# Kernel tuning notes

Measured on AMD Instinct MI355X. Metric: run time of the kernel, lower is better.

Reference implementation:

```python
import jax, jax.numpy as jnp
import numpy as np

L, D, H, N = 9, 256, 4, 1024
DH = D // H          # head dim = 64
FH = DH // 2         # fourier half dim = 32


def _lin(x, W, b):
    return x @ W + b


def _ln(x, g, b, eps=1e-5):
    mu = jnp.mean(x, -1, keepdims=True)
    var = jnp.mean((x - mu) ** 2, -1, keepdims=True)
    return (x - mu) * jax.lax.rsqrt(var + eps) * g + b


def _ffn(x, m, W1, b1, g, beta, W2, b2):
    h = jax.nn.gelu(_ln(_lin(jnp.concatenate([x, m], -1), W1, b1), g, beta), approximate=False)
    return x + _lin(h, W2, b2)


def _rotate_half(x):
    x1, x2 = x[..., 0::2], x[..., 1::2]
    return jnp.stack((-x2, x1), -1).reshape(x.shape)


def _rope(f, t):
    return t * f[0] + _rotate_half(t) * f[1]


def _posenc(kpts, Wr):
    proj = kpts @ Wr                                   # [b,n,FH]
    emb = jnp.stack([jnp.cos(proj), jnp.sin(proj)], 0)  # [2,b,n,FH]
    emb = jnp.repeat(emb, 2, axis=3)                    # [2,b,n,DH]
    return emb[:, None]                                 # [2,1,b,n,DH]


def _heads(t):
    b, n, _ = t.shape
    return t.reshape(b, n, H, DH).transpose(0, 2, 1, 3)


def _merge(t):
    b, h, n, d = t.shape
    return t.transpose(0, 2, 1, 3).reshape(b, n, h * d)


def _self_block(x, enc, Wqkv, bqkv, Wo, bo, fp):
    b, n, _ = x.shape
    qkv = _lin(x, Wqkv, bqkv).reshape(b, n, H, DH, 3).transpose(0, 2, 1, 3, 4)
    q, k, v = qkv[..., 0], qkv[..., 1], qkv[..., 2]
    q, k = _rope(enc, q), _rope(enc, k)
    attn = jax.nn.softmax(jnp.einsum('bhid,bhjd->bhij', q, k) * DH ** -0.5, -1)
    msg = _lin(_merge(jnp.einsum('bhij,bhjd->bhid', attn, v)), Wo, bo)
    return _ffn(x, msg, *fp)


def _cross_block(x0, x1, Wqk, bqk, Wv, bv, Wo, bo, fp):
    s = DH ** -0.25
    qk0 = _heads(_lin(x0, Wqk, bqk)) * s
    qk1 = _heads(_lin(x1, Wqk, bqk)) * s
    v0, v1 = _heads(_lin(x0, Wv, bv)), _heads(_lin(x1, Wv, bv))
    sim = jnp.einsum('bhid,bhjd->bhij', qk0, qk1)       # shared similarity
    m0 = jnp.einsum('bhij,bhjd->bhid', jax.nn.softmax(sim, -1), v1)
    m1 = jnp.einsum('bhij,bhid->bhjd', jax.nn.softmax(sim, -2), v0)
    m0, m1 = _lin(_merge(m0), Wo, bo), _lin(_merge(m1), Wo, bo)
    return _ffn(x0, m0, *fp), _ffn(x1, m1, *fp)


def _assignment(d0, d1, Wp, bp, Wz, bz):
    s = D ** -0.25
    md0, md1 = _lin(d0, Wp, bp) * s, _lin(d1, Wp, bp) * s
    sim = jnp.einsum('bmd,bnd->bmn', md0, md1)
    z0 = d0 @ Wz + bz[:1]                               # [b,m,1]
    z1 = d1 @ Wz + bz[:1]                               # [b,n,1]
    cert = jax.nn.log_sigmoid(z0) + jnp.swapaxes(jax.nn.log_sigmoid(z1), 1, 2)
    inner = jax.nn.log_softmax(sim, -1) + jax.nn.log_softmax(sim, -2) + cert
    col = jax.nn.log_sigmoid(-z0)                       # [b,m,1]
    row = jnp.swapaxes(jax.nn.log_sigmoid(-z1), 1, 2)   # [b,1,n]
    top = jnp.concatenate([inner, col], 2)
    bot = jnp.concatenate([row, jnp.zeros_like(row[:, :, :1])], 2)
    return jnp.concatenate([top, bot], 1)               # [b,m+1,n+1]


def _forward(desc0, desc1, kpts0, kpts1, Wr,
             sWqkv, sbqkv, sWo, sbo, sfW1, sfb1, sfg, sfbeta, sfW2, sfb2,
             cWqk, cbqk, cWv, cbv, cWo, cbo, cfW1, cfb1, cfg, cfbeta, cfW2, cfb2,
             mWp, mbp, mWz, mbz):
    enc0, enc1 = _posenc(kpts0, Wr), _posenc(kpts1, Wr)
    for i in range(L):
        sfp = (sfW1[i], sfb1[i], sfg[i], sfbeta[i], sfW2[i], sfb2[i])
        cfp = (cfW1[i], cfb1[i], cfg[i], cfbeta[i], cfW2[i], cfb2[i])
        desc0 = _self_block(desc0, enc0, sWqkv[i], sbqkv[i], sWo[i], sbo[i], sfp)
        desc1 = _self_block(desc1, enc1, sWqkv[i], sbqkv[i], sWo[i], sbo[i], sfp)
        desc0, desc1 = _cross_block(desc0, desc1, cWqk[i], cbqk[i], cWv[i], cbv[i], cWo[i], cbo[i], cfp)
    return _assignment(desc0, desc1, mWp, mbp, mWz, mbz)


def setup_inputs() -> dict:
    key = jax.random.key(0)
    ks = iter(jax.random.split(key, 64))

    def nrm(shape, std=0.02):
        return std * jax.random.normal(next(ks), shape, jnp.float32)

    return {
        'desc0': nrm((1, N, D), 1.0), 'desc1': nrm((1, N, D), 1.0),
        'kpts0': nrm((1, N, 2), 1.0), 'kpts1': nrm((1, N, 2), 1.0),
        'Wr': nrm((2, FH), 1.0),
        'sWqkv': nrm((L, D, 3 * D)), 'sbqkv': jnp.zeros((L, 3 * D), jnp.float32),
        'sWo': nrm((L, D, D)), 'sbo': jnp.zeros((L, D), jnp.float32),
        'sfW1': nrm((L, 2 * D, 2 * D)), 'sfb1': jnp.zeros((L, 2 * D), jnp.float32),
        'sfg': jnp.ones((L, 2 * D), jnp.float32), 'sfbeta': jnp.zeros((L, 2 * D), jnp.float32),
        'sfW2': nrm((L, 2 * D, D)), 'sfb2': jnp.zeros((L, D), jnp.float32),
        'cWqk': nrm((L, D, D)), 'cbqk': jnp.zeros((L, D), jnp.float32),
        'cWv': nrm((L, D, D)), 'cbv': jnp.zeros((L, D), jnp.float32),
        'cWo': nrm((L, D, D)), 'cbo': jnp.zeros((L, D), jnp.float32),
        'cfW1': nrm((L, 2 * D, 2 * D)), 'cfb1': jnp.zeros((L, 2 * D), jnp.float32),
        'cfg': jnp.ones((L, 2 * D), jnp.float32), 'cfbeta': jnp.zeros((L, 2 * D), jnp.float32),
        'cfW2': nrm((L, 2 * D, D)), 'cfb2': jnp.zeros((L, D), jnp.float32),
        'mWp': nrm((D, D)), 'mbp': jnp.zeros((D,), jnp.float32),
        'mWz': nrm((D, 1)), 'mbz': jnp.zeros((D,), jnp.float32),
    }


def reference(desc0, desc1, kpts0, kpts1, Wr,
              sWqkv, sbqkv, sWo, sbo, sfW1, sfb1, sfg, sfbeta, sfW2, sfb2,
              cWqk, cbqk, cWv, cbv, cWo, cbo, cfW1, cfb1, cfg, cfbeta, cfW2, cfb2,
              mWp, mbp, mWz, mbz):
    return _forward(desc0, desc1, kpts0, kpts1, Wr,
                    sWqkv, sbqkv, sWo, sbo, sfW1, sfb1, sfg, sfbeta, sfW2, sfb2,
                    cWqk, cbqk, cWv, cbv, cWo, cbo, cfW1, cfb1, cfg, cfbeta, cfW2, cfb2,
                    mWp, mbp, mWz, mbz)
```

## Files before the change

kernel.cpp:

```cpp
#include <hip/hip_runtime.h>
#include <cmath>

#define NTOK 1024
#define DM   256
#define NH   4
#define DH   64
#define NL   9

typedef __attribute__((ext_vector_type(8))) __bf16 bf16x8;
typedef __attribute__((ext_vector_type(4))) __bf16 bf16x4;
typedef __attribute__((ext_vector_type(4))) float  f32x4;

__device__ __forceinline__ float logsigf(float x) {
    return fminf(x, 0.0f) - log1pf(expf(-fabsf(x)));
}

__device__ __forceinline__ __bf16 f2bf(float f) {
    unsigned u = __float_as_uint(f);
    u = (u + 0x7FFFu + ((u >> 16) & 1u)) >> 16;
    unsigned short s = (unsigned short)u;
    return __builtin_bit_cast(__bf16, s);
}

__global__ __launch_bounds__(256) void wtrans_all_k(
    const float* __restrict__ sWqkv, const float* __restrict__ sWo,
    const float* __restrict__ sfW1,  const float* __restrict__ sfW2,
    const float* __restrict__ cWqk,  const float* __restrict__ cWv,
    const float* __restrict__ cWo,   const float* __restrict__ cfW1,
    const float* __restrict__ cfW2,  const float* __restrict__ mWp,
    __bf16* __restrict__ wb)
{
    const int z = blockIdx.z;
    const float* src; __bf16* dst; int K, N, b;
    if      (z <  9) { src = sWqkv; dst = wb;            K = 256; N = 768; b = z;      }
    else if (z < 18) { src = sWo;   dst = wb + 1769472;  K = 256; N = 256; b = z - 9;  }
    else if (z < 27) { src = sfW1;  dst = wb + 2359296;  K = 512; N = 512; b = z - 18; }
    else if (z < 36) { src = sfW2;  dst = wb + 4718592;  K = 512; N = 256; b = z - 27; }
    else if (z < 45) { src = cWqk;  dst = wb + 5898240;  K = 256; N = 256; b = z - 36; }
    else if (z < 54) { src = cWv;   dst = wb + 6488064;  K = 256; N = 256; b = z - 45; }
    else if (z < 63) { src = cWo;   dst = wb + 7077888;  K = 256; N = 256; b = z - 54; }
    else if (z < 72) { src = cfW1;  dst = wb + 7667712;  K = 512; N = 512; b = z - 63; }
    else if (z < 81) { src = cfW2;  dst = wb + 10027008; K = 512; N = 256; b = z - 72; }
    else             { src = mWp;   dst = wb + 11206656; K = 256; N = 256; b = 0;      }
    const int n0 = blockIdx.x * 32, k0 = blockIdx.y * 32;
    if (n0 >= N || k0 >= K) return;
    src += (size_t)b * K * N;
    dst += (size_t)b * K * N;

    __shared__ __bf16 t[32][36];
    const int tx = threadIdx.x & 31, ty = threadIdx.x >> 5;
    #pragma unroll
    for (int i = 0; i < 4; ++i) {
        int k = ty + i * 8;
        t[tx][k] = f2bf(src[(size_t)(k0 + k) * N + n0 + tx]);
    }
    __syncthreads();
    const int nr = threadIdx.x >> 3, kc = (threadIdx.x & 7) * 4;
    bf16x4 v = *(const bf16x4*)&t[nr][kc];
    int outr = n0 + nr;
    if (z < 9) {
        int h = outr / 192, r = outr % 192;
        outr = (r % 3) * 256 + h * 64 + (r / 3);
    }
    *(bf16x4*)&dst[(size_t)outr * K + k0 + kc] = v;
}

__global__ __launch_bounds__(256) void wfuse_k(
    const __bf16* __restrict__ tW1s, const __bf16* __restrict__ tWos,
    const __bf16* __restrict__ tW1c, const __bf16* __restrict__ tWoc,
    __bf16* __restrict__ tW1f)
{
    const int z = blockIdx.z, bx = blockIdx.x, tid = threadIdx.x;
    const __bf16* A  = (z < 9) ? tW1s + (size_t)z * 262144 : tW1c + (size_t)(z - 9) * 262144;
    const __bf16* B  = (z < 9) ? tWos + (size_t)z * 65536  : tWoc + (size_t)(z - 9) * 65536;
    __bf16* dst      = tW1f + (size_t)z * 262144;
    const int row0 = blockIdx.y * 32;

    if (bx < 4) {
        const int row = tid >> 3, kc = (tid & 7) * 8;
        bf16x8 v = *(const bf16x8*)&A[(size_t)(row0 + row) * 512 + bx * 64 + kc];
        *(bf16x8*)&dst[(size_t)(row0 + row) * 512 + bx * 64 + kc] = v;
        return;
    }

    __shared__ __bf16 As[8][32][40];
    __shared__ __bf16 Bs[8][64][40];
    const int w = tid >> 6, l = tid & 63;
    const int col0 = (bx - 4) * 64;
    const int wr = (w >> 1) * 16, wc = (w & 1) * 32;
    f32x4 acc0 = {0.f, 0.f, 0.f, 0.f};
    f32x4 acc1 = {0.f, 0.f, 0.f, 0.f};

    const int ar = tid >> 3, ac = (tid & 7) * 4;
    const int tnr = tid >> 3, tkc = (tid & 7) * 8;

    #pragma unroll
    for (int c = 0; c < 8; ++c) {
        bf16x4 av = *(const bf16x4*)&A[(size_t)(row0 + ar) * 512 + 256 + c * 32 + ac];
        *(bf16x4*)&As[c][ar][ac] = av;
        bf16x8 bv = *(const bf16x8*)&B[(size_t)(c * 32 + tnr) * 256 + col0 + tkc];
        #pragma unroll
        for (int e = 0; e < 8; ++e) Bs[c][tkc + e][tnr] = bv[e];
    }
    __syncthreads();
    #pragma unroll
    for (int c = 0; c < 8; ++c) {
        bf16x8 af  = *(const bf16x8*)&As[c][wr + (l & 15)][(l >> 4) * 8];
        bf16x8 bf0 = *(const bf16x8*)&Bs[c][wc + (l & 15)][(l >> 4) * 8];
        bf16x8 bf1 = *(const bf16x8*)&Bs[c][wc + 16 + (l & 15)][(l >> 4) * 8];
        acc0 = __builtin_amdgcn_mfma_f32_16x16x32_bf16(af, bf0, acc0, 0, 0, 0);
        acc1 = __builtin_amdgcn_mfma_f32_16x16x32_bf16(af, bf1, acc1, 0, 0, 0);
    }
    #pragma unroll
    for (int t2 = 0; t2 < 2; ++t2) {
        f32x4 a = t2 ? acc1 : acc0;
        int cc = col0 + wc + t2 * 16 + (l & 15);
        #pragma unroll
        for (int rg = 0; rg < 4; ++rg) {
            int rr = row0 + wr + (l >> 4) * 4 + rg;
            dst[(size_t)rr * 512 + 256 + cc] = f2bf(a[rg]);
        }
    }
}

__global__ __launch_bounds__(256) void bfuse_k(
    const float* __restrict__ sbo, const float* __restrict__ sfW1,
    const float* __restrict__ sfb1, const float* __restrict__ cbo,
    const float* __restrict__ cfW1, const float* __restrict__ cfb1,
    float* __restrict__ bf)
{
    const int z = blockIdx.y;
    const float* bo = (z < 9) ? sbo + z * 256 : cbo + (z - 9) * 256;
    const float* W1 = (z < 9) ? sfW1 + (size_t)z * 262144 : cfW1 + (size_t)(z - 9) * 262144;
    const float* b1 = (z < 9) ? sfb1 + z * 512 : cfb1 + (z - 9) * 512;
    const int o = blockIdx.x * 256 + threadIdx.x;
    float acc = 0.f;
    for (int m = 0; m < 256; ++m)
        acc += bo[m] * W1[(size_t)(256 + m) * 512 + o];
    bf[(size_t)z * 512 + o] = b1[o] + acc;
}

__global__ __launch_bounds__(256) void gemm_qkv_k(
    const __bf16* __restrict__ Ab, const __bf16* __restrict__ Bt,
    const float* __restrict__ bias,
    const float* __restrict__ encc, const float* __restrict__ encs,
    __bf16* __restrict__ qh, __bf16* __restrict__ kh, __bf16* __restrict__ vh)
{
    __shared__ __bf16 As[8][32][40];
    __shared__ __bf16 Bs[8][64][40];
    const int tid = threadIdx.x;
    const int w = tid >> 6, l = tid & 63;
    const int row0 = blockIdx.y * 32, col0 = blockIdx.x * 64;
    const int wr = (w >> 1) * 16, wc = (w & 1) * 32;
    const int quad = l >> 4, l16 = l & 15;
    f32x4 acc0 = {0.f, 0.f, 0.f, 0.f};
    f32x4 acc1 = {0.f, 0.f, 0.f, 0.f};

    const int ar = tid >> 3, ac = (tid & 7) * 4;
    const int bnr = tid >> 2, bkc = (tid & 3) * 8;

    #pragma unroll
    for (int c = 0; c < 8; ++c) {
        const int k0 = c * 32;
        bf16x4 av = *(const bf16x4*)&Ab[(size_t)(row0 + ar) * 256 + k0 + ac];
        *(bf16x4*)&As[c][ar][ac] = av;
        bf16x8 bv = *(const bf16x8*)&Bt[(size_t)(col0 + bnr) * 256 + k0 + bkc];
        *(bf16x8*)&Bs[c][bnr][bkc] = bv;
    }
    __syncthreads();
    #pragma unroll
    for (int c = 0; c < 8; ++c) {
        bf16x8 af  = *(const bf16x8*)&As[c][wr + l16][quad * 8];
        bf16x8 bf0 = *(const bf16x8*)&Bs[c][wc + l16][quad * 8];
        bf16x8 bf1 = *(const bf16x8*)&Bs[c][wc + 16 + l16][quad * 8];
        acc0 = __builtin_amdgcn_mfma_f32_16x16x32_bf16(af, bf0, acc0, 0, 0, 0);
        acc1 = __builtin_amdgcn_mfma_f32_16x16x32_bf16(af, bf1, acc1, 0, 0, 0);
    }

    const int typ = col0 >> 8;
    const int hh  = (col0 & 255) >> 6;
    __bf16* dst = (typ == 0) ? qh : (typ == 1) ? kh : vh;
    #pragma unroll
    for (int t2 = 0; t2 < 2; ++t2) {
        f32x4 a = t2 ? acc1 : acc0;
        const int d = wc + t2 * 16 + l16;
        const float bvv = bias[hh * 192 + d * 3 + typ];
        float full[4], pair[4];
        #pragma unroll
        for (int rg = 0; rg < 4; ++rg) full[rg] = a[rg] + bvv;
        #pragma unroll
        for (int rg = 0; rg < 4; ++rg) pair[rg] = __shfl_xor(full[rg], 1);
        const float sgn = (d & 1) ? 1.0f : -1.0f;
        #pragma unroll
        for (int rg = 0; rg < 4; ++rg) {
            int rr = row0 + wr + quad * 4 + rg;
            float outv;
            if (typ == 2) {
                outv = full[rg];
            } else {
                float c = encc[(size_t)rr * 64 + d];
                float s = encs[(size_t)rr * 64 + d];
                outv = full[rg] * c + sgn * pair[rg] * s;
            }
            int im = rr >> 10, n = rr & 1023;
            dst[(((size_t)(im * 4 + hh)) * 1024 + n) * 64 + d] = f2bf(outv);
        }
    }
}

__global__ __launch_bounds__(256) void gemm_bf_k(
    const __bf16* __restrict__ Ab, const __bf16* __restrict__ A1b,
    const __bf16* __restrict__ Bt, const float* __restrict__ bias,
    float* __restrict__ C, int K, int Nn, int ldc, float scale)
{
    __shared__ __bf16 As[8][32][40];
    __shared__ __bf16 Bs[8][64][40];
    const int tid = threadIdx.x;
    const int w = tid >> 6, l = tid & 63;
    const int row0 = blockIdx.y * 32, col0 = blockIdx.x * 64;
    const int wr = (w >> 1) * 16, wc = (w & 1) * 32;
    f32x4 acc0 = {0.f, 0.f, 0.f, 0.f};
    f32x4 acc1 = {0.f, 0.f, 0.f, 0.f};

    const int ar = tid >> 3, ac = (tid & 7) * 4;
    const int bnr = tid >> 2, bkc = (tid & 3) * 8;

    for (int p0 = 0; p0 < K; p0 += 256) {
        #pragma unroll
        for (int c = 0; c < 8; ++c) {
            const int k0 = p0 + c * 32;
            const int kk = k0 + ac;
            const __bf16* src = (A1b && kk >= 256)
                ? &A1b[(size_t)(row0 + ar) * 256 + (kk - 256)]
                : &Ab[(size_t)(row0 + ar) * 256 + kk];
            bf16x4 av = *(const bf16x4*)src;
            *(bf16x4*)&As[c][ar][ac] = av;
            bf16x8 bv = *(const bf16x8*)&Bt[(size_t)(col0 + bnr) * K + k0 + bkc];
            *(bf16x8*)&Bs[c][bnr][bkc] = bv;
        }
        __syncthreads();
        #pragma unroll
        for (int c = 0; c < 8; ++c) {
            bf16x8 af  = *(const bf16x8*)&As[c][wr + (l & 15)][(l >> 4) * 8];
            bf16x8 bf0 = *(const bf16x8*)&Bs[c][wc + (l & 15)][(l >> 4) * 8];
            bf16x8 bf1 = *(const bf16x8*)&Bs[c][wc + 16 + (l & 15)][(l >> 4) * 8];
            acc0 = __builtin_amdgcn_mfma_f32_16x16x32_bf16(af, bf0, acc0, 0, 0, 0);
            acc1 = __builtin_amdgcn_mfma_f32_16x16x32_bf16(af, bf1, acc1, 0, 0, 0);
        }
        __syncthreads();
    }

    #pragma unroll
    for (int t2 = 0; t2 < 2; ++t2) {
        f32x4 a = t2 ? acc1 : acc0;
        int cc = col0 + wc + t2 * 16 + (l & 15);
        float bvv = bias ? bias[cc] : 0.0f;
        #pragma unroll
        for (int rg = 0; rg < 4; ++rg) {
            int rr = row0 + wr + (l >> 4) * 4 + rg;
            C[(size_t)rr * ldc + cc] = (a[rg] + bvv) * scale;
        }
    }
}

__global__ __launch_bounds__(256) void gemm_bfb_k(
    const __bf16* __restrict__ Ab, const __bf16* __restrict__ Bt,
    const float* __restrict__ bias, __bf16* __restrict__ Cb, float scale)
{
    __shared__ __bf16 As[8][32][40];
    __shared__ __bf16 Bs[8][64][40];
    const int tid = threadIdx.x;
    const int w = tid >> 6, l = tid & 63;
    const int row0 = blockIdx.y * 32, col0 = blockIdx.x * 64;
    const int wr = (w >> 1) * 16, wc = (w & 1) * 32;
    f32x4 acc0 = {0.f, 0.f, 0.f, 0.f};
    f32x4 acc1 = {0.f, 0.f, 0.f, 0.f};

    const int ar = tid >> 3, ac = (tid & 7) * 4;
    const int bnr = tid >> 2, bkc = (tid & 3) * 8;

    #pragma unroll
    for (int c = 0; c < 8; ++c) {
        const int k0 = c * 32;
        bf16x4 av = *(const bf16x4*)&Ab[(size_t)(row0 + ar) * 256 + k0 + ac];
        *(bf16x4*)&As[c][ar][ac] = av;
        bf16x8 bv = *(const bf16x8*)&Bt[(size_t)(col0 + bnr) * 256 + k0 + bkc];
        *(bf16x8*)&Bs[c][bnr][bkc] = bv;
    }
    __syncthreads();
    #pragma unroll
    for (int c = 0; c < 8; ++c) {
        bf16x8 af  = *(const bf16x8*)&As[c][wr + (l & 15)][(l >> 4) * 8];
        bf16x8 bf0 = *(const bf16x8*)&Bs[c][wc + (l & 15)][(l >> 4) * 8];
        bf16x8 bf1 = *(const bf16x8*)&Bs[c][wc + 16 + (l & 15)][(l >> 4) * 8];
        acc0 = __builtin_amdgcn_mfma_f32_16x16x32_bf16(af, bf0, acc0, 0, 0, 0);
        acc1 = __builtin_amdgcn_mfma_f32_16x16x32_bf16(af, bf1, acc1, 0, 0, 0);
    }

    #pragma unroll
    for (int t2 = 0; t2 < 2; ++t2) {
        f32x4 a = t2 ? acc1 : acc0;
        int cc = col0 + wc + t2 * 16 + (l & 15);
        float bvv = bias[cc];
        #pragma unroll
        for (int rg = 0; rg < 4; ++rg) {
            int rr = row0 + wr + (l >> 4) * 4 + rg;
            Cb[(size_t)rr * 256 + cc] = f2bf((a[rg] + bvv) * scale);
        }
    }
}

__global__ __launch_bounds__(256) void ffn2f_k(
    const float* __restrict__ pre, const float* __restrict__ g,
    const float* __restrict__ beta, const __bf16* __restrict__ Bt,
    const float* __restrict__ bias, float* __restrict__ x,
    __bf16* __restrict__ xb)
{
    __shared__ __bf16 hAs[2][8][16][40];
    const int tid = threadIdx.x;
    const int r = tid >> 4, sub = tid & 15;
    const int row0 = blockIdx.x * 16;

    float v[32];
    const float* pr = pre + (size_t)(row0 + r) * 512 + sub * 32;
    float s = 0.f;
    #pragma unroll
    for (int j4 = 0; j4 < 8; ++j4) {
        float4 t = *(const float4*)&pr[j4 * 4];
        v[j4 * 4 + 0] = t.x; v[j4 * 4 + 1] = t.y;
        v[j4 * 4 + 2] = t.z; v[j4 * 4 + 3] = t.w;
        s += t.x + t.y + t.z + t.w;
    }
    #pragma unroll
    for (int ofs = 1; ofs < 16; ofs <<= 1) s += __shfl_xor(s, ofs);
    const float mu = s * (1.0f / 512.0f);
    float ss = 0.f;
    #pragma unroll
    for (int j = 0; j < 32; ++j) { float d = v[j] - mu; ss += d * d; }
    #pragma unroll
    for (int ofs = 1; ofs < 16; ofs <<= 1) ss += __shfl_xor(ss, ofs);
    const float rstd = rsqrtf(ss * (1.0f / 512.0f) + 1e-5f);

    const int p = sub >> 3, c = sub & 7;
    const float IS2 = 0.70710678118654752f;
    bf16x8 hb8[4];
    #pragma unroll
    for (int j4 = 0; j4 < 8; ++j4) {
        float4 gg = *(const float4*)&g[sub * 32 + j4 * 4];
        float4 bb = *(const float4*)&beta[sub * 32 + j4 * 4];
        float y;
        y = (v[j4*4+0] - mu) * rstd * gg.x + bb.x;
        hb8[j4 >> 1][(j4 & 1) * 4 + 0] = f2bf(0.5f * y * (1.0f + erff(y * IS2)));
        y = (v[j4*4+1] - mu) * rstd * gg.y + bb.y;
        hb8[j4 >> 1][(j4 & 1) * 4 + 1] = f2bf(0.5f * y * (1.0f + erff(y * IS2)));
        y = (v[j4*4+2] - mu) * rstd * gg.z + bb.z;
        hb8[j4 >> 1][(j4 & 1) * 4 + 2] = f2bf(0.5f * y * (1.0f + erff(y * IS2)));
        y = (v[j4*4+3] - mu) * rstd * gg.w + bb.w;
        hb8[j4 >> 1][(j4 & 1) * 4 + 3] = f2bf(0.5f * y * (1.0f + erff(y * IS2)));
    }
    #pragma unroll
    for (int j8 = 0; j8 < 4; ++j8)
        *(bf16x8*)&hAs[p][c][r][j8 * 8] = hb8[j8];
    __syncthreads();

    const int w = tid >> 6, l = tid & 63;
    const int quad = l >> 4, l16 = l & 15;
    f32x4 acc0 = {0.f, 0.f, 0.f, 0.f};
    f32x4 acc1 = {0.f, 0.f, 0.f, 0.f};
    f32x4 acc2 = {0.f, 0.f, 0.f, 0.f};
    f32x4 acc3 = {0.f, 0.f, 0.f, 0.f};
    const size_t bcol = (size_t)(w * 64 + l16) * 512;
    #pragma unroll
    for (int p2 = 0; p2 < 2; ++p2) {
        #pragma unroll
        for (int c2 = 0; c2 < 8; ++c2) {
            bf16x8 af = *(const bf16x8*)&hAs[p2][c2][l16][quad * 8];
            const size_t kofs = p2 * 256 + c2 * 32 + quad * 8;
            bf16x8 b0 = *(const bf16x8*)&Bt[bcol + kofs];
            bf16x8 b1 = *(const bf16x8*)&Bt[bcol + 16 * 512 + kofs];
            bf16x8 b2 = *(const bf16x8*)&Bt[bcol + 32 * 512 + kofs];
            bf16x8 b3 = *(const bf16x8*)&Bt[bcol + 48 * 512 + kofs];
            acc0 = __builtin_amdgcn_mfma_f32_16x16x32_bf16(af, b0, acc0, 0, 0, 0);
            acc1 = __builtin_amdgcn_mfma_f32_16x16x32_bf16(af, b1, acc1, 0, 0, 0);
            acc2 = __builtin_amdgcn_mfma_f32_16x16x32_bf16(af, b2, acc2, 0, 0, 0);
            acc3 = __builtin_amdgcn_mfma_f32_16x16x32_bf16(af, b3, acc3, 0, 0, 0);
        }
    }

    #pragma unroll
    for (int f = 0; f < 4; ++f) {
        f32x4 a = (f == 0) ? acc0 : (f == 1) ? acc1 : (f == 2) ? acc2 : acc3;
        int cc = w * 64 + f * 16 + l16;
        float bvv = bias[cc];
        #pragma unroll
        for (int rg = 0; rg < 4; ++rg) {
            int rr = row0 + quad * 4 + rg;
            float outv = a[rg] + bvv + x[(size_t)rr * 256 + cc];
            x[(size_t)rr * 256 + cc]  = outv;
            xb[(size_t)rr * 256 + cc] = f2bf(outv);
        }
    }
}

__global__ __launch_bounds__(256) void gemm_hm2_k(
    const __bf16* __restrict__ Ab, const __bf16* __restrict__ Btq,
    const float* __restrict__ bq, const __bf16* __restrict__ Btv,
    const float* __restrict__ bv, __bf16* __restrict__ outq,
    __bf16* __restrict__ outv, float scaleq)
{
    const int bx = blockIdx.x;
    const __bf16* Bt  = (bx < 4) ? Btq : Btv;
    const float* bias = (bx < 4) ? bq : bv;
    __bf16* C         = (bx < 4) ? outq : outv;
    const float scale = (bx < 4) ? scaleq : 1.0f;

    __shared__ __bf16 As[8][32][40];
    __shared__ __bf16 Bs[8][64][40];
    const int tid = threadIdx.x;
    const int w = tid >> 6, l = tid & 63;
    const int row0 = blockIdx.y * 32, col0 = (bx & 3) * 64;
    const int wr = (w >> 1) * 16, wc = (w & 1) * 32;
    f32x4 acc0 = {0.f, 0.f, 0.f, 0.f};
    f32x4 acc1 = {0.f, 0.f, 0.f, 0.f};

    const int ar = tid >> 3, ac = (tid & 7) * 4;
    const int bnr = tid >> 2, bkc = (tid & 3) * 8;

    #pragma unroll
    for (int c = 0; c < 8; ++c) {
        const int k0 = c * 32;
        bf16x4 av = *(const bf16x4*)&Ab[(size_t)(row0 + ar) * 256 + k0 + ac];
        *(bf16x4*)&As[c][ar][ac] = av;
        bf16x8 bv8 = *(const bf16x8*)&Bt[(size_t)(col0 + bnr) * 256 + k0 + bkc];
        *(bf16x8*)&Bs[c][bnr][bkc] = bv8;
    }
    __syncthreads();
    #pragma unroll
    for (int c = 0; c < 8; ++c) {
        bf16x8 af  = *(const bf16x8*)&As[c][wr + (l & 15)][(l >> 4) * 8];
        bf16x8 bf0 = *(const bf16x8*)&Bs[c][wc + (l & 15)][(l >> 4) * 8];
        bf16x8 bf1 = *(const bf16x8*)&Bs[c][wc + 16 + (l & 15)][(l >> 4) * 8];
        acc0 = __builtin_amdgcn_mfma_f32_16x16x32_bf16(af, bf0, acc0, 0, 0, 0);
        acc1 = __builtin_amdgcn_mfma_f32_16x16x32_bf16(af, bf1, acc1, 0, 0, 0);
    }

    #pragma unroll
    for (int t2 = 0; t2 < 2; ++t2) {
        f32x4 a = t2 ? acc1 : acc0;
        int cc = col0 + wc + t2 * 16 + (l & 15);
        float bvv = bias ? bias[cc] : 0.0f;
        int h = cc >> 6, d = cc & 63;
        #pragma unroll
        for (int rg = 0; rg < 4; ++rg) {
            int rr = row0 + wr + (l >> 4) * 4 + rg;
            int im = rr >> 10, n = rr & 1023;
            C[(((size_t)(im * 4 + h)) * 1024 + n) * 64 + d] = f2bf((a[rg] + bvv) * scale);
        }
    }
}

__global__ __launch_bounds__(256) void gemm_bt_k(
    const __bf16* __restrict__ Ab, const __bf16* __restrict__ Bb,
    float* __restrict__ C, int Nn)
{
    __shared__ __bf16 As[8][32][40];
    __shared__ __bf16 Bs[8][64][40];
    const int tid = threadIdx.x;
    const int w = tid >> 6, l = tid & 63;
    const int row0 = blockIdx.y * 32, col0 = blockIdx.x * 64;
    const int wr = (w >> 1) * 16, wc = (w & 1) * 32;
    f32x4 acc0 = {0.f, 0.f, 0.f, 0.f};
    f32x4 acc1 = {0.f, 0.f, 0.f, 0.f};

    const int ar = tid >> 3, ac = (tid & 7) * 4;
    const int bnr = tid >> 2, bkc = (tid & 3) * 8;

    #pragma unroll
    for (int c = 0; c < 8; ++c) {
        const int k0 = c * 32;
        bf16x4 av = *(const bf16x4*)&Ab[(size_t)(row0 + ar) * 256 + k0 + ac];
        *(bf16x4*)&As[c][ar][ac] = av;
        bf16x8 bv = *(const bf16x8*)&Bb[(size_t)(col0 + bnr) * 256 + k0 + bkc];
        *(bf16x8*)&Bs[c][bnr][bkc] = bv;
    }
    __syncthreads();
    #pragma unroll
    for (int c = 0; c < 8; ++c) {
        bf16x8 af  = *(const bf16x8*)&As[c][wr + (l & 15)][(l >> 4) * 8];
        bf16x8 bf0 = *(const bf16x8*)&Bs[c][wc + (l & 15)][(l >> 4) * 8];
        bf16x8 bf1 = *(const bf16x8*)&Bs[c][wc + 16 + (l & 15)][(l >> 4) * 8];
        acc0 = __builtin_amdgcn_mfma_f32_16x16x32_bf16(af, bf0, acc0, 0, 0, 0);
        acc1 = __builtin_amdgcn_mfma_f32_16x16x32_bf16(af, bf1, acc1, 0, 0, 0);
    }

    #pragma unroll
    for (int t2 = 0; t2 < 2; ++t2) {
        f32x4 a = t2 ? acc1 : acc0;
        int cc = col0 + wc + t2 * 16 + (l & 15);
        #pragma unroll
        for (int rg = 0; rg < 4; ++rg) {
            int rr = row0 + wr + (l >> 4) * 4 + rg;
            C[(size_t)rr * Nn + cc] = a[rg];
        }
    }
}

__global__ __launch_bounds__(256) void init_k(
    const float* __restrict__ desc0, const float* __restrict__ desc1,
    const float* __restrict__ kpts0, const float* __restrict__ kpts1,
    const float* __restrict__ Wr, float* __restrict__ x,
    __bf16* __restrict__ xb,
    float* __restrict__ encc, float* __restrict__ encs)
{
    int idx = blockIdx.x * 256 + threadIdx.x;
    if (idx < 524288) {
        float v = (idx < 262144) ? desc0[idx] : desc1[idx - 262144];
        x[idx]  = v;
        xb[idx] = f2bf(v);
    } else {
        int p = idx - 524288;
        int im = p >> 15, q = p & 32767;
        int i = q >> 5, f = q & 31;
        const float* kp = im ? kpts1 : kpts0;
        float* ec = encc + im * 65536;
        float* es = encs + im * 65536;
        float pr = kp[i * 2] * Wr[f] + kp[i * 2 + 1] * Wr[32 + f];
        float c = cosf(pr), s = sinf(pr);
        ec[i * 64 + 2 * f] = c; ec[i * 64 + 2 * f + 1] = c;
        es[i * 64 + 2 * f] = s; es[i * 64 + 2 * f + 1] = s;
    }
}

__global__ __launch_bounds__(256) void attn_k(
    const __bf16* __restrict__ Qg, const __bf16* __restrict__ Kg,
    const __bf16* __restrict__ Vg, __bf16* __restrict__ out,
    float scale, int cross)
{
    const int qt = blockIdx.x, hv = blockIdx.y;
    const int kvh = cross ? (hv ^ 4) : hv;
    const int tid = threadIdx.x;
    const int w = tid >> 6, lane = tid & 63;
    const int quad = lane >> 4, l16 = lane & 15;
    const int n0 = qt * 16;

    __shared__ __align__(16) char smem[44032];
    char* base = smem + w * 11008;
    __bf16* kb  = (__bf16*)(base);
    __bf16* vtb = (__bf16*)(base + 4608);
    __bf16* ptb = (__bf16*)(base + 9728);

    bf16x8 qf[2];
    {
        const bf16x8* Qp = (const bf16x8*)(Qg + (((size_t)hv * 1024) + n0 + l16) * 64);
        qf[0] = Qp[quad];
        qf[1] = Qp[4 + quad];
    }

    const __bf16* Kbase = Kg + (size_t)kvh * 1024 * 64;
    const __bf16* Vbase = Vg + (size_t)kvh * 1024 * 64;

    float m[4] = {-1e30f, -1e30f, -1e30f, -1e30f};
    float lsum[4] = {0.f, 0.f, 0.f, 0.f};
    f32x4 o[4] = {{0,0,0,0},{0,0,0,0},{0,0,0,0},{0,0,0,0}};

    const int kj = lane >> 1, kd = (lane & 1) * 32;
    const int vjp = lane & 15, vd0 = (lane >> 4) * 16;

    bf16x8 kr[4];
    uint4  vr[4];
    {
        const int j0 = w * 256;
        const bf16x8* kp = (const bf16x8*)(Kbase + (size_t)(j0 + kj) * 64 + kd);
        kr[0] = kp[0]; kr[1] = kp[1]; kr[2] = kp[2]; kr[3] = kp[3];
        const uint4* va = (const uint4*)(Vbase + (size_t)(j0 + 2 * vjp) * 64 + vd0);
        const uint4* vb = (const uint4*)(Vbase + (size_t)(j0 + 2 * vjp + 1) * 64 + vd0);
        vr[0] = va[0]; vr[1] = va[1]; vr[2] = vb[0]; vr[3] = vb[1];
    }

    for (int t = 0; t < 8; ++t) {
        {
            __bf16* krow = kb + kj * 72 + kd;
            *(bf16x8*)(krow)      = kr[0];
            *(bf16x8*)(krow + 8)  = kr[1];
            *(bf16x8*)(krow + 16) = kr[2];
            *(bf16x8*)(krow + 24) = kr[3];
            #pragma unroll
            for (int g = 0; g < 2; ++g) {
                uint4 ua = vr[g], ub = vr[2 + g];
                unsigned au[4] = {ua.x, ua.y, ua.z, ua.w};
                unsigned bu[4] = {ub.x, ub.y, ub.z, ub.w};
                #pragma unroll
                for (int e = 0; e < 4; ++e) {
                    int i = g * 8 + e * 2;
                    unsigned pk0 = ((bu[e] & 0xFFFFu) << 16) | (au[e] & 0xFFFFu);
                    unsigned pk1 = (bu[e] & 0xFFFF0000u) | (au[e] >> 16);
                    *(unsigned*)((char*)vtb + ((vd0 + i) * 40 + 2 * vjp) * 2)     = pk0;
                    *(unsigned*)((char*)vtb + ((vd0 + i + 1) * 40 + 2 * vjp) * 2) = pk1;
                }
            }
        }
        if (t < 7) {
            const int j1 = w * 256 + (t + 1) * 32;
            const bf16x8* kp = (const bf16x8*)(Kbase + (size_t)(j1 + kj) * 64 + kd);
            kr[0] = kp[0]; kr[1] = kp[1]; kr[2] = kp[2]; kr[3] = kp[3];
            const uint4* va = (const uint4*)(Vbase + (size_t)(j1 + 2 * vjp) * 64 + vd0);
            const uint4* vb = (const uint4*)(Vbase + (size_t)(j1 + 2 * vjp + 1) * 64 + vd0);
            vr[0] = va[0]; vr[1] = va[1]; vr[2] = vb[0]; vr[3] = vb[1];
        }

        f32x4 s0 = {0,0,0,0}, s1 = {0,0,0,0};
        #pragma unroll
        for (int kt = 0; kt < 2; ++kt) {
            bf16x8 k0 = *(const bf16x8*)(kb + (0 * 16 + l16) * 72 + kt * 32 + quad * 8);
            bf16x8 k1 = *(const bf16x8*)(kb + (1 * 16 + l16) * 72 + kt * 32 + quad * 8);
            s0 = __builtin_amdgcn_mfma_f32_16x16x32_bf16(qf[kt], k0, s0, 0, 0, 0);
            s1 = __builtin_amdgcn_mfma_f32_16x16x32_bf16(qf[kt], k1, s1, 0, 0, 0);
        }

        float rm[4], p0[4], p1[4], rs[4];
        #pragma unroll
        for (int r = 0; r < 4; ++r) {
            s0[r] *= scale; s1[r] *= scale;
            rm[r] = fmaxf(s0[r], s1[r]);
        }
        #pragma unroll
        for (int ofs = 1; ofs < 16; ofs <<= 1)
            #pragma unroll
            for (int r = 0; r < 4; ++r)
                rm[r] = fmaxf(rm[r], __shfl_xor(rm[r], ofs));
        #pragma unroll
        for (int r = 0; r < 4; ++r) {
            float mn = fmaxf(m[r], rm[r]);
            float alpha = __expf(m[r] - mn);
            m[r] = mn;
            p0[r] = __expf(s0[r] - mn);
            p1[r] = __expf(s1[r] - mn);
            rs[r] = p0[r] + p1[r];
            lsum[r] *= alpha;
            #pragma unroll
            for (int dt = 0; dt < 4; ++dt) o[dt][r] *= alpha;
        }
        #pragma unroll
        for (int ofs = 1; ofs < 16; ofs <<= 1)
            #pragma unroll
            for (int r = 0; r < 4; ++r)
                rs[r] += __shfl_xor(rs[r], ofs);
        #pragma unroll
        for (int r = 0; r < 4; ++r) lsum[r] += rs[r];

        #pragma unroll
        for (int r = 0; r < 4; ++r) {
            ptb[(quad * 4 + r) * 40 + l16]      = f2bf(p0[r]);
            ptb[(quad * 4 + r) * 40 + 16 + l16] = f2bf(p1[r]);
        }
        bf16x8 pf = *(const bf16x8*)(ptb + l16 * 40 + quad * 8);
        #pragma unroll
        for (int dt = 0; dt < 4; ++dt) {
            bf16x8 vf = *(const bf16x8*)(vtb + (dt * 16 + l16) * 40 + quad * 8);
            o[dt] = __builtin_amdgcn_mfma_f32_16x16x32_bf16(pf, vf, o[dt], 0, 0, 0);
        }
    }

    __syncthreads();
    float* Om = (float*)smem;
    float* mm = Om + 4096;
    float* lm = mm + 64;
    #pragma unroll
    for (int dt = 0; dt < 4; ++dt)
        #pragma unroll
        for (int r = 0; r < 4; ++r)
            Om[(w * 16 + quad * 4 + r) * 64 + dt * 16 + l16] = o[dt][r];
    if (l16 == 0) {
        #pragma unroll
        for (int r = 0; r < 4; ++r) {
            mm[w * 16 + quad * 4 + r] = m[r];
            lm[w * 16 + quad * 4 + r] = lsum[r];
        }
    }
    __syncthreads();

    const int q = tid >> 4, dg = tid & 15;
    float M = -1e30f;
    #pragma unroll
    for (int w2 = 0; w2 < 4; ++w2) M = fmaxf(M, mm[w2 * 16 + q]);
    float L = 0.f;
    float4 acc = {0.f, 0.f, 0.f, 0.f};
    #pragma unroll
    for (int w2 = 0; w2 < 4; ++w2) {
        float e = __expf(mm[w2 * 16 + q] - M);
        L += e * lm[w2 * 16 + q];
        float4 ov = *(const float4*)&Om[(w2 * 16 + q) * 64 + dg * 4];
        acc.x += e * ov.x; acc.y += e * ov.y; acc.z += e * ov.z; acc.w += e * ov.w;
    }
    float inv = 1.0f / L;
    bf16x4 ob;
    ob[0] = f2bf(acc.x * inv); ob[1] = f2bf(acc.y * inv);
    ob[2] = f2bf(acc.z * inv); ob[3] = f2bf(acc.w * inv);
    int row = (hv >> 2) * 1024 + n0 + q;
    *(bf16x4*)&out[(size_t)row * 256 + (hv & 3) * 64 + dg * 4] = ob;
}

__global__ __launch_bounds__(256) void z_k(
    const float* __restrict__ x, const float* __restrict__ Wz,
    const float* __restrict__ bz, float* __restrict__ z)
{
    int row = blockIdx.x * 4 + (threadIdx.x >> 6);
    int lane = threadIdx.x & 63;
    float4 v  = *(const float4*)&x[(size_t)row * 256 + lane * 4];
    float4 wv = *(const float4*)&Wz[lane * 4];
    float s = v.x * wv.x + v.y * wv.y + v.z * wv.z + v.w * wv.w;
    #pragma unroll
    for (int ofs = 1; ofs < 64; ofs <<= 1) s += __shfl_xor(s, ofs);
    if (lane == 0) z[row] = s + bz[0];
}

__global__ __launch_bounds__(256) void lse_k(
    const float* __restrict__ sim, float* __restrict__ rls,
    float* __restrict__ cls)
{
    const int b = blockIdx.x, t = threadIdx.x;
    const int isCol = b >> 10, rc = b & 1023;
    const size_t base = isCol ? (size_t)rc : (size_t)rc * 1024;
    const size_t stride = isCol ? 1024 : 1;
    __shared__ float red[256];
    float mx = -1e30f;
    for (int j = t; j < NTOK; j += 256) mx = fmaxf(mx, sim[base + stride * j]);
    red[t] = mx; __syncthreads();
    for (int s = 128; s > 0; s >>= 1) {
        if (t < s) red[t] = fmaxf(red[t], red[t + s]);
        __syncthreads();
    }
    mx = red[0]; __syncthreads();
    float sum = 0.0f;
    for (int j = t; j < NTOK; j += 256) sum += expf(sim[base + stride * j] - mx);
    red[t] = sum; __syncthreads();
    for (int s = 128; s > 0; s >>= 1) {
        if (t < s) red[t] += red[t + s];
        __syncthreads();
    }
    if (t == 0) (isCol ? cls : rls)[rc] = mx + logf(red[0]);
}

__global__ __launch_bounds__(256) void assemble_k(
    const float* __restrict__ sim, const float* __restrict__ rls,
    const float* __restrict__ cls, const float* __restrict__ z0,
    const float* __restrict__ z1, float* __restrict__ out)
{
    int idx = blockIdx.x * 256 + threadIdx.x;
    const int W = NTOK + 1;
    if (idx >= W * W) return;
    int i = idx / W, j = idx % W;
    float v;
    if (i < NTOK && j < NTOK) {
        v = 2.0f * sim[(size_t)i * NTOK + j] - rls[i] - cls[j] + logsigf(z0[i]) + logsigf(z1[j]);
    } else if (i < NTOK) {
        v = logsigf(-z0[i]);
    } else if (j < NTOK) {
        v = logsigf(-z1[j]);
    } else {
        v = 0.0f;
    }
    out[idx] = v;
}

extern "C" void kernel_launch(void* const* d_in, const int* in_sizes, int n_in,
                              void* d_out, int out_size, void* d_ws, size_t ws_size,
                              hipStream_t stream)
{
    const float* desc0 = (const float*)d_in[0];
    const float* desc1 = (const float*)d_in[1];
    const float* kpts0 = (const float*)d_in[2];
    const float* kpts1 = (const float*)d_in[3];
    const float* Wr    = (const float*)d_in[4];
    const float* sWqkv = (const float*)d_in[5];
    const float* sbqkv = (const float*)d_in[6];
    const float* sWo   = (const float*)d_in[7];
    const float* sbo   = (const float*)d_in[8];
    const float* sfW1  = (const float*)d_in[9];
    const float* sfb1  = (const float*)d_in[10];
    const float* sfg   = (const float*)d_in[11];
    const float* sfbt  = (const float*)d_in[12];
    const float* sfW2  = (const float*)d_in[13];
    const float* sfb2  = (const float*)d_in[14];
    const float* cWqk  = (const float*)d_in[15];
    const float* cbqk  = (const float*)d_in[16];
    const float* cWv   = (const float*)d_in[17];
    const float* cbv   = (const float*)d_in[18];
    const float* cWo   = (const float*)d_in[19];
    const float* cbo   = (const float*)d_in[20];
    const float* cfW1  = (const float*)d_in[21];
    const float* cfb1  = (const float*)d_in[22];
    const float* cfg   = (const float*)d_in[23];
    const float* cfbt  = (const float*)d_in[24];
    const float* cfW2  = (const float*)d_in[25];
    const float* cfb2  = (const float*)d_in[26];
    const float* mWp   = (const float*)d_in[27];
    const float* mbp   = (const float*)d_in[28];
    const float* mWz   = (const float*)d_in[29];
    const float* mbz   = (const float*)d_in[30];

    float* ws = (float*)d_ws;
    float*  x    = ws;
    float*  encc = ws + 524288;
    float*  encs = ws + 655360;
    float*  pre  = ws + 786432;
    __bf16* qh   = (__bf16*)(ws + 2359296);
    __bf16* kh   = (__bf16*)(ws + 2621440);
    __bf16* vh   = (__bf16*)(ws + 2883584);
    __bf16* msgb = (__bf16*)(ws + 3145728);
    float*  zb   = ws + 3276800;
    float*  rlsb = ws + 3278848;
    float*  clsb = ws + 3279872;
    float*  sim  = pre;
    __bf16* mdb  = (__bf16*)(ws + 1835008);

    __bf16* wb    = (__bf16*)(ws + 3280896);
    __bf16* tWqkv = wb;
    __bf16* tWo   = tWqkv + 1769472;
    __bf16* tW1   = tWo   + 589824;
    __bf16* tW2   = tW1   + 2359296;
    __bf16* tcQk  = tW2   + 1179648;
    __bf16* tcV   = tcQk  + 589824;
    __bf16* tcWo  = tcV   + 589824;
    __bf16* tcW1  = tcWo  + 589824;
    __bf16* tcW2  = tcW1  + 2359296;
    __bf16* tmWp  = tcW2  + 1179648;
    __bf16* tW1f  = (__bf16*)(ws + 8916992);
    float*  bfb   = ws + 11276288;
    __bf16* xb    = (__bf16*)(ws + 11285504);

    wtrans_all_k<<<dim3(24, 16, 82), 256, 0, stream>>>(
        sWqkv, sWo, sfW1, sfW2, cWqk, cWv, cWo, cfW1, cfW2, mWp, wb);
    wfuse_k<<<dim3(8, 16, 18), 256, 0, stream>>>(tW1, tWo, tcW1, tcWo, tW1f);
    bfuse_k<<<dim3(2, 18), 256, 0, stream>>>(sbo, sfW1, sfb1, cbo, cfW1, cfb1, bfb);

    const float SELF_SCALE  = 0.125f;
    const float CROSS_SCALE = 0.35355339059327373f;

    init_k<<<2304, 256, 0, stream>>>(desc0, desc1, kpts0, kpts1, Wr, x, xb, encc, encs);

    for (int l = 0; l < NL; ++l) {
        gemm_qkv_k<<<dim3(12, 64), 256, 0, stream>>>(
            xb, tWqkv + (size_t)l * 196608, sbqkv + (size_t)l * 768,
            encc, encs, qh, kh, vh);
        attn_k<<<dim3(64, 8), 256, 0, stream>>>(qh, kh, vh, msgb, SELF_SCALE, 0);
        gemm_bf_k<<<dim3(8, 64), 256, 0, stream>>>(
            xb, msgb, tW1f + (size_t)l * 262144, bfb + (size_t)l * 512,
            pre, 512, 512, 512, 1.0f);
        ffn2f_k<<<128, 256, 0, stream>>>(
            pre, sfg + (size_t)l * 512, sfbt + (size_t)l * 512,
            tW2 + (size_t)l * 131072, sfb2 + (size_t)l * 256, x, xb);

        gemm_hm2_k<<<dim3(8, 64), 256, 0, stream>>>(
            xb, tcQk + (size_t)l * 65536, cbqk + (size_t)l * 256,
            tcV + (size_t)l * 65536, cbv + (size_t)l * 256,
            qh, vh, CROSS_SCALE);
        attn_k<<<dim3(64, 8), 256, 0, stream>>>(qh, qh, vh, msgb, 1.0f, 1);
        gemm_bf_k<<<dim3(8, 64), 256, 0, stream>>>(
            xb, msgb, tW1f + (size_t)(9 + l) * 262144, bfb + (size_t)(9 + l) * 512,
            pre, 512, 512, 512, 1.0f);
        ffn2f_k<<<128, 256, 0, stream>>>(
            pre, cfg + (size_t)l * 512, cfbt + (size_t)l * 512,
            tcW2 + (size_t)l * 131072, cfb2 + (size_t)l * 256, x, xb);
    }

    const float MD_SCALE = 0.25f;
    gemm_bfb_k<<<dim3(4, 64), 256, 0, stream>>>(xb, tmWp, mbp, mdb, MD_SCALE);
    z_k<<<512, 256, 0, stream>>>(x, mWz, mbz, zb);
    gemm_bt_k<<<dim3(16, 32), 256, 0, stream>>>(mdb, mdb + 1024 * 256, sim, 1024);
    lse_k<<<2048, 256, 0, stream>>>(sim, rlsb, clsb);
    const int W = NTOK + 1;
    assemble_k<<<(W * W + 255) / 256, 256, 0, stream>>>(sim, rlsb, clsb, zb, zb + 1024, (float*)d_out);
}
```

Measured before the change: 1.110 ms.

## Split FFN2 fused kernel across output columns and stage weights in LDS

The fused LayerNorm+GELU+second-FFN-GEMM kernel now uses a 2D grid of 4 column tiles by 128 row tiles instead of 128 blocks, so 512 blocks run instead of 128. Each block computes a 16x64 output tile and stages weight tiles through shared memory with barriers, rather than each wave reading weights straight from global memory. The cost is that LayerNorm and GELU over the full 512-wide row are recomputed four times, once per column block.

```diff
diff --git a/kernel.cpp b/kernel.cpp
--- a/kernel.cpp
+++ b/kernel.cpp
@@ -310,17 +310,18 @@
     }
 }
 
-__global__ __launch_bounds__(256) void ffn2f_k(
+__global__ __launch_bounds__(256) void ffn3_k(
     const float* __restrict__ pre, const float* __restrict__ g,
     const float* __restrict__ beta, const __bf16* __restrict__ Bt,
     const float* __restrict__ bias, float* __restrict__ x,
     __bf16* __restrict__ xb)
 {
-    __shared__ __bf16 hAs[2][8][16][40];
+    __shared__ __bf16 As[2][8][16][40];
+    __shared__ __bf16 Bs[8][64][40];
     const int tid = threadIdx.x;
+    const int row0 = blockIdx.y * 16, col0 = blockIdx.x * 64;
+
     const int r = tid >> 4, sub = tid & 15;
-    const int row0 = blockIdx.x * 16;
-
     float v[32];
     const float* pr = pre + (size_t)(row0 + r) * 512 + sub * 32;
     float s = 0.f;
@@ -343,59 +344,56 @@
 
     const int p = sub >> 3, c = sub & 7;
     const float IS2 = 0.70710678118654752f;
-    bf16x8 hb8[4];
-    #pragma unroll
-    for (int j4 = 0; j4 < 8; ++j4) {
-        float4 gg = *(const float4*)&g[sub * 32 + j4 * 4];
-        float4 bb = *(const float4*)&beta[sub * 32 + j4 * 4];
-        float y;
-        y = (v[j4*4+0] - mu) * rstd * gg.x + bb.x;
-        hb8[j4 >> 1][(j4 & 1) * 4 + 0] = f2bf(0.5f * y * (1.0f + erff(y * IS2)));
-        y = (v[j4*4+1] - mu) * rstd * gg.y + bb.y;
-        hb8[j4 >> 1][(j4 & 1) * 4 + 1] = f2bf(0.5f * y * (1.0f + erff(y * IS2)));
-        y = (v[j4*4+2] - mu) * rstd * gg.z + bb.z;
-        hb8[j4 >> 1][(j4 & 1) * 4 + 2] = f2bf(0.5f * y * (1.0f + erff(y * IS2)));
-        y = (v[j4*4+3] - mu) * rstd * gg.w + bb.w;
-        hb8[j4 >> 1][(j4 & 1) * 4 + 3] = f2bf(0.5f * y * (1.0f + erff(y * IS2)));
-    }
-    #pragma unroll
-    for (int j8 = 0; j8 < 4; ++j8)
-        *(bf16x8*)&hAs[p][c][r][j8 * 8] = hb8[j8];
-    __syncthreads();
+    #pragma unroll
+    for (int j8 = 0; j8 < 4; ++j8) {
+        bf16x8 hb;
+        #pragma unroll
+        for (int e4 = 0; e4 < 2; ++e4) {
+            float4 gg = *(const float4*)&g[sub * 32 + j8 * 8 + e4 * 4];
+            float4 bb = *(const float4*)&beta[sub * 32 + j8 * 8 + e4 * 4];
+            int j = j8 * 8 + e4 * 4;
+            float y;
+            y = (v[j+0] - mu) * rstd * gg.x + bb.x;
+            hb[e4*4+0] = f2bf(0.5f * y * (1.0f + erff(y * IS2)));
+            y = (v[j+1] - mu) * rstd * gg.y + bb.y;
+            hb[e4*4+1] = f2bf(0.5f * y * (1.0f + erff(y * IS2)));
+            y = (v[j+2] - mu) * rstd * gg.z + bb.z;
+            hb[e4*4+2] = f2bf(0.5f * y * (1.0f + erff(y * IS2)));
+            y = (v[j+3] - mu) * rstd * gg.w + bb.w;
+            hb[e4*4+3] = f2bf(0.5f * y * (1.0f + erff(y * IS2)));
+        }
+        *(bf16x8*)&As[p][c][r][j8 * 8] = hb;
+    }
 
     const int w = tid >> 6, l = tid & 63;
     const int quad = l >> 4, l16 = l & 15;
-    f32x4 acc0 = {0.f, 0.f, 0.f, 0.f};
-    f32x4 acc1 = {0.f, 0.f, 0.f, 0.f};
-    f32x4 acc2 = {0.f, 0.f, 0.f, 0.f};
-    f32x4 acc3 = {0.f, 0.f, 0.f, 0.f};
-    const size_t bcol = (size_t)(w * 64 + l16) * 512;
-    #pragma unroll
+    f32x4 acc = {0.f, 0.f, 0.f, 0.f};
+    const int bnr = tid >> 2, bkc = (tid & 3) * 8;
+
     for (int p2 = 0; p2 < 2; ++p2) {
         #pragma unroll
         for (int c2 = 0; c2 < 8; ++c2) {
-            bf16x8 af = *(const bf16x8*)&hAs[p2][c2][l16][quad * 8];
-            const size_t kofs = p2 * 256 + c2 * 32 + quad * 8;
-            bf16x8 b0 = *(const bf16x8*)&Bt[bcol + kofs];
-            bf16x8 b1 = *(const bf16x8*)&Bt[bcol + 16 * 512 + kofs];
-            bf16x8 b2 = *(const bf16x8*)&Bt[bcol + 32 * 512 + kofs];
-            bf16x8 b3 = *(const bf16x8*)&Bt[bcol + 48 * 512 + kofs];
-            acc0 = __builtin_amdgcn_mfma_f32_16x16x32_bf16(af, b0, acc0, 0, 0, 0);
-            acc1 = __builtin_amdgcn_mfma_f32_16x16x32_bf16(af, b1, acc1, 0, 0, 0);
-            acc2 = __builtin_amdgcn_mfma_f32_16x16x32_bf16(af, b2, acc2, 0, 0, 0);
-            acc3 = __builtin_amdgcn_mfma_f32_16x16x32_bf16(af, b3, acc3, 0, 0, 0);
-        }
-    }
-
-    #pragma unroll
-    for (int f = 0; f < 4; ++f) {
-        f32x4 a = (f == 0) ? acc0 : (f == 1) ? acc1 : (f == 2) ? acc2 : acc3;
-        int cc = w * 64 + f * 16 + l16;
+            const int k0 = p2 * 256 + c2 * 32;
+            bf16x8 bv = *(const bf16x8*)&Bt[(size_t)(col0 + bnr) * 512 + k0 + bkc];
+            *(bf16x8*)&Bs[c2][bnr][bkc] = bv;
+        }
+        __syncthreads();
+        #pragma unroll
+        for (int c2 = 0; c2 < 8; ++c2) {
+            bf16x8 af = *(const bf16x8*)&As[p2][c2][l16][quad * 8];
+            bf16x8 bf = *(const bf16x8*)&Bs[c2][w * 16 + l16][quad * 8];
+            acc = __builtin_amdgcn_mfma_f32_16x16x32_bf16(af, bf, acc, 0, 0, 0);
+        }
+        __syncthreads();
+    }
+
+    {
+        int cc = col0 + w * 16 + l16;
         float bvv = bias[cc];
         #pragma unroll
         for (int rg = 0; rg < 4; ++rg) {
             int rr = row0 + quad * 4 + rg;
-            float outv = a[rg] + bvv + x[(size_t)rr * 256 + cc];
+            float outv = acc[rg] + bvv + x[(size_t)rr * 256 + cc];
             x[(size_t)rr * 256 + cc]  = outv;
             xb[(size_t)rr * 256 + cc] = f2bf(outv);
         }
@@ -847,7 +845,7 @@
         gemm_bf_k<<<dim3(8, 64), 256, 0, stream>>>(
             xb, msgb, tW1f + (size_t)l * 262144, bfb + (size_t)l * 512,
             pre, 512, 512, 512, 1.0f);
-        ffn2f_k<<<128, 256, 0, stream>>>(
+        ffn3_k<<<dim3(4, 128), 256, 0, stream>>>(
             pre, sfg + (size_t)l * 512, sfbt + (size_t)l * 512,
             tW2 + (size_t)l * 131072, sfb2 + (size_t)l * 256, x, xb);
 
@@ -859,7 +857,7 @@
         gemm_bf_k<<<dim3(8, 64), 256, 0, stream>>>(
             xb, msgb, tW1f + (size_t)(9 + l) * 262144, bfb + (size_t)(9 + l) * 512,
             pre, 512, 512, 512, 1.0f);
-        ffn2f_k<<<128, 256, 0, stream>>>(
+        ffn3_k<<<dim3(4, 128), 256, 0, stream>>>(
             pre, cfg + (size_t)l * 512, cfbt + (size_t)l * 512,
             tcW2 + (size_t)l * 131072, cfb2 + (size_t)l * 256, x, xb);
     }
```

Result: faster. 968.5 us (-12.8%).
